# Optimization experiments

Hardware: AMD Instinct MI355X
Metric: run time of the kernel (lower is better)

Reference implementation:

```python
import jax, jax.numpy as jnp
import numpy as np
import math

IMG_SIZE = 768
NUM_CLASSES = 90
THRESHOLD = 0.05
IOU_THRESHOLD = 0.5
MAX_DETECTIONS = 100
K_CAND = 512  # per-class candidate pool before greedy NMS
RATIOS = [(1.0, 1.0), (1.4, 0.7), (0.7, 1.4)]
SCALES = [2 ** 0, 2 ** (1.0 / 3.0), 2 ** (2.0 / 3.0)]


def _generate_anchors():
    anchor_scale = 4.0
    pyramid_levels = [3, 4, 5, 6, 7]
    all_levels = []
    for lv in pyramid_levels:
        stride = 2 ** lv
        size = anchor_scale * 2 ** lv
        grid = IMG_SIZE // stride
        sx = np.arange(grid) * stride
        sy, sx = np.meshgrid(np.arange(grid) * stride, sx, indexing='ij')
        # torch meshgrid(shift_y, shift_x, indexing='ij') -> rows are y
        yy, xx = np.meshgrid(np.arange(grid) * stride, np.arange(grid) * stride, indexing='ij')
        shifts = np.stack([xx.ravel(), yy.ravel(), xx.ravel(), yy.ravel()], axis=1).astype(np.float32)
        base = []
        for r in RATIOS:
            for s in SCALES:
                w = size * s * math.sqrt(r[0] / r[1])
                h = size * s * math.sqrt(r[1] / r[0])
                base.append([-w / 2, -h / 2, w / 2, h / 2])
        base = np.asarray(base, dtype=np.float32)  # [9,4]
        anc = (base[None, :, :] + shifts[:, None, :]).reshape(-1, 4)
        all_levels.append(anc)
    return np.concatenate(all_levels, axis=0)  # [110484,4]


def setup_inputs() -> dict:
    key = jax.random.key(0)
    k1, k2, k3 = jax.random.split(key, 3)
    A = 110484
    x = jax.random.normal(k1, (1, 3, IMG_SIZE, IMG_SIZE), dtype=jnp.float32)
    regression = jax.random.normal(k2, (1, A, 4), dtype=jnp.float32) * 0.3
    classification = jax.random.normal(k3, (1, A, NUM_CLASSES), dtype=jnp.float32) - 2.0
    anchors = jnp.asarray(_generate_anchors())
    return {"x": x, "regression": regression, "classification": classification, "anchors": anchors}


def _decode_and_clip(anchors, deltas, H, W):
    # BBoxTransform (RetinaNet-style): deltas = (dx, dy, dw, dh)
    wa = anchors[:, 2] - anchors[:, 0]
    ha = anchors[:, 3] - anchors[:, 1]
    cxa = anchors[:, 0] + 0.5 * wa
    cya = anchors[:, 1] + 0.5 * ha
    dx, dy, dw, dh = deltas[:, 0], deltas[:, 1], deltas[:, 2], deltas[:, 3]
    cx = cxa + dx * wa
    cy = cya + dy * ha
    w = jnp.exp(dw) * wa
    h = jnp.exp(dh) * ha
    x1 = jnp.clip(cx - 0.5 * w, 0.0, W)
    y1 = jnp.clip(cy - 0.5 * h, 0.0, H)
    x2 = jnp.clip(cx + 0.5 * w, 0.0, W)
    y2 = jnp.clip(cy + 0.5 * h, 0.0, H)
    return jnp.stack([x1, y1, x2, y2], axis=1)  # [A,4]


def _pairwise_iou(b):  # [K,4] -> [K,K]
    area = (b[:, 2] - b[:, 0]) * (b[:, 3] - b[:, 1])
    xx1 = jnp.maximum(b[:, None, 0], b[None, :, 0])
    yy1 = jnp.maximum(b[:, None, 1], b[None, :, 1])
    xx2 = jnp.minimum(b[:, None, 2], b[None, :, 2])
    yy2 = jnp.minimum(b[:, None, 3], b[None, :, 3])
    inter = jnp.clip(xx2 - xx1, 0.0) * jnp.clip(yy2 - yy1, 0.0)
    return inter / (area[:, None] + area[None, :] - inter + 1e-8)


def _greedy_nms(iou_c, valid_c):
    # boxes are pre-sorted by descending score; fixed-iteration greedy NMS
    def step(suppressed, i):
        keep_i = valid_c[i] & jnp.logical_not(suppressed[i])
        suppressed = jnp.where(keep_i, suppressed | (iou_c[i] > IOU_THRESHOLD), suppressed)
        return suppressed, keep_i
    _, keep = jax.lax.scan(step, jnp.zeros(iou_c.shape[0], dtype=bool), jnp.arange(iou_c.shape[0]))
    return keep  # [K]


def _postprocess(x, regression, classification, anchors):
    H, W = x.shape[2], x.shape[3]
    boxes = _decode_and_clip(anchors, regression[0], float(H), float(W))  # [A,4]
    scores = jax.nn.sigmoid(classification[0])                            # [A,C]
    # per-class top-K candidate pool (sorted desc), fixed-shape NMS
    vals, idx = jax.lax.top_k(scores.T, K_CAND)        # [C,K]
    cand = boxes[idx]                                   # [C,K,4]
    valid = vals > THRESHOLD                            # [C,K]
    iou = jax.vmap(_pairwise_iou)(cand)                 # [C,K,K]
    keep = jax.vmap(_greedy_nms)(iou, valid)            # [C,K]
    kept_scores = jnp.where(keep, vals, -1.0).reshape(-1)  # [C*K]
    top_vals, flat_idx = jax.lax.top_k(kept_scores, MAX_DETECTIONS)
    labels = (flat_idx // K_CAND).astype(jnp.float32)
    det_boxes = cand.reshape(-1, 4)[flat_idx]
    ok = top_vals > 0.0
    det = jnp.concatenate([
        jnp.zeros((MAX_DETECTIONS, 1), dtype=jnp.float32),  # batch ids (batch=1 -> 0)
        det_boxes,
        top_vals[:, None],
        labels[:, None],
    ], axis=1)  # [100,7]
    return jnp.where(ok[:, None], det, 0.0)


def reference(x, regression, classification, anchors):
    return _postprocess(x, regression, classification, anchors)
```

## Files before the change

### kernel.cpp

```cpp
#include <hip/hip_runtime.h>
#include <math.h>


#define A_N   110484
#define C_N   90
#define KCAND 512
#define NBINS 8192
#define KSH   19
#define MAXDET 100
#define IMG_F 768.0f
#define THRESH 0.05f
#define NS    4
#define VTOT  (A_N / 4)
#define VS4   ((VTOT + NS - 1) / NS)
#define SL_CAP 1024
#define CAND_N (NS * KCAND)
#define KEEP_CAP 100
#define T_BLKS ((A_N + 63) / 64)
#define S_BLKS (C_N * NS)
#define D_BLKS ((A_N + 255) / 256)
#define FCAP  512

typedef unsigned int u32;
typedef unsigned long long u64;

__device__ __forceinline__ u32 fkey(float f) {
    u32 u = __float_as_uint(f);
    return (u & 0x80000000u) ? ~u : (u | 0x80000000u);
}
__device__ __forceinline__ float unfkey(u32 k) {
    u32 u = (k & 0x80000000u) ? (k ^ 0x80000000u) : ~k;
    return __uint_as_float(u);
}
__device__ __forceinline__ u64 shflx64(u64 v, int m) {
    u32 lo = (u32)__shfl_xor((int)(u32)v, m, 64);
    u32 hi = (u32)__shfl_xor((int)(v >> 32), m, 64);
    return ((u64)hi << 32) | lo;
}

__global__ __launch_bounds__(256)
void prep_kernel(const float* __restrict__ cls,
                 u32* __restrict__ keysT) {
    __shared__ u32 tile[64 * 91];
    const int a0 = blockIdx.x * 64;
    const int lim = min(64, A_N - a0);
    const int n4 = (lim * C_N) >> 2;
    const float4* src4 = (const float4*)(cls + (size_t)a0 * C_N);
    for (int i4 = threadIdx.x; i4 < n4; i4 += 256) {
        float4 x4 = src4[i4];
        const u32 base = (u32)(4 * i4);
        float xs[4] = { x4.x, x4.y, x4.z, x4.w };
        #pragma unroll
        for (int k = 0; k < 4; ++k) {
            u32 i = base + k;
            u32 aa = i / C_N, c = i % C_N;
            float s = 1.0f / (1.0f + expf(-xs[k]));
            tile[aa * 91 + c] = fkey(s);
        }
    }
    __syncthreads();
    for (int j = threadIdx.x; j < C_N * 64; j += 256) {
        int c = j >> 6, aa = j & 63;
        if (aa < lim)
            keysT[(size_t)c * A_N + a0 + aa] = tile[aa * 91 + c];
    }
}

__global__ __launch_bounds__(256)
void select_kernel(const u32* __restrict__ keysT,
                   const float* __restrict__ anchors,
                   const float* __restrict__ reg,
                   float4* __restrict__ boxes,
                   u64* __restrict__ candbuf) {
    __shared__ u32 hist[NBINS];
    __shared__ u32 csum[256];
    __shared__ u64 lbuf[SL_CAP];
    __shared__ u32 sPv;
    __shared__ int lcnt;
    const int tid = threadIdx.x;

    if (blockIdx.x >= S_BLKS) {
        int a = (blockIdx.x - S_BLKS) * 256 + tid;
        if (a < A_N) {
            float4 an = ((const float4*)anchors)[a];
            float4 dl = ((const float4*)reg)[a];
            float wa = an.z - an.x, ha = an.w - an.y;
            float cx = an.x + 0.5f * wa + dl.x * wa;
            float cy = an.y + 0.5f * ha + dl.y * ha;
            float w = expf(dl.z) * wa;
            float h = expf(dl.w) * ha;
            float4 o;
            o.x = fminf(fmaxf(cx - 0.5f * w, 0.0f), IMG_F);
            o.y = fminf(fmaxf(cy - 0.5f * h, 0.0f), IMG_F);
            o.z = fminf(fmaxf(cx + 0.5f * w, 0.0f), IMG_F);
            o.w = fminf(fmaxf(cy + 0.5f * h, 0.0f), IMG_F);
            boxes[a] = o;
        }
        return;
    }
    const int c = blockIdx.x >> 2, s = blockIdx.x & 3;
    const int lo = s * VS4, hiEnd = min(VTOT, lo + VS4);
    const uint4* kv = (const uint4*)(keysT + (size_t)c * A_N);

    for (int i = tid; i < NBINS; i += 256) hist[i] = 0;
    if (tid == 0) { sPv = 0; lcnt = 0; }
    __syncthreads();
    for (int i = lo + tid; i < hiEnd; i += 256) {
        uint4 k = kv[i];
        atomicAdd(&hist[k.x >> KSH], 1u);
        atomicAdd(&hist[k.y >> KSH], 1u);
        atomicAdd(&hist[k.z >> KSH], 1u);
        atomicAdd(&hist[k.w >> KSH], 1u);
    }
    __syncthreads();
    u32 own = 0; const int hi = NBINS - 1 - 32 * tid;
    #pragma unroll 4
    for (int j = 0; j < 32; ++j) own += hist[hi - j];
    csum[tid] = own;
    __syncthreads();
    for (int off = 1; off < 256; off <<= 1) {
        u32 v = csum[tid];
        u32 a = (tid >= off) ? csum[tid - off] : 0u;
        __syncthreads();
        csum[tid] = v + a;
        __syncthreads();
    }
    const u32 incl = csum[tid], excl = incl - own;
    if (excl < (u32)KCAND && incl >= (u32)KCAND) {
        u32 cum = excl;
        for (int j = 0; j < 32; ++j) {
            u32 hv = hist[hi - j];
            if (cum + hv >= (u32)KCAND) { sPv = (u32)(hi - j); break; }
            cum += hv;
        }
    }
    __syncthreads();
    const u32 P = sPv;
    for (int i = lo + tid; i < hiEnd; i += 256) {
        uint4 k = kv[i];
        u32 base = (u32)(4 * i);
        if ((k.x >> KSH) >= P) {
            int p = atomicAdd(&lcnt, 1);
            if (p < SL_CAP) lbuf[p] = (((u64)(~k.x)) << 32) | base;
        }
        if ((k.y >> KSH) >= P) {
            int p = atomicAdd(&lcnt, 1);
            if (p < SL_CAP) lbuf[p] = (((u64)(~k.y)) << 32) | (base + 1);
        }
        if ((k.z >> KSH) >= P) {
            int p = atomicAdd(&lcnt, 1);
            if (p < SL_CAP) lbuf[p] = (((u64)(~k.z)) << 32) | (base + 2);
        }
        if ((k.w >> KSH) >= P) {
            int p = atomicAdd(&lcnt, 1);
            if (p < SL_CAP) lbuf[p] = (((u64)(~k.w)) << 32) | (base + 3);
        }
    }
    __syncthreads();
    const int n = min(lcnt, SL_CAP);
    for (int i = tid; i < SL_CAP; i += 256) if (i >= n) lbuf[i] = ~0ULL;
    __syncthreads();

    {
        const int l = tid & 63, w = tid >> 6;
        int ii[4]; u64 v[4];
        #pragma unroll
        for (int r = 0; r < 4; ++r) { ii[r] = 256 * w + 64 * r + l; v[r] = lbuf[ii[r]]; }
        __syncthreads();
        #pragma unroll
        for (u32 kk = 2; kk <= 1024; kk <<= 1) {
            #pragma unroll
            for (u32 j = kk >> 1; j > 0; j >>= 1) {
                if (j >= 256) {
                    #pragma unroll
                    for (int r = 0; r < 4; ++r) lbuf[ii[r]] = v[r];
                    __syncthreads();
                    #pragma unroll
                    for (int r = 0; r < 4; ++r) {
                        u64 pv = lbuf[ii[r] ^ j];
                        bool up = ((ii[r] & kk) == 0);
                        bool m = (((ii[r] & j) == 0) == up);
                        v[r] = m ? (v[r] < pv ? v[r] : pv) : (v[r] > pv ? v[r] : pv);
                    }
                    __syncthreads();
                } else if (j >= 64) {
                    const int rx = (int)(j >> 6);
                    u64 nv[4];
                    #pragma unroll
                    for (int r = 0; r < 4; ++r) {
                        u64 pv = v[r ^ rx];
                        bool up = ((ii[r] & kk) == 0);
                        bool m = (((ii[r] & j) == 0) == up);
                        nv[r] = m ? (v[r] < pv ? v[r] : pv) : (v[r] > pv ? v[r] : pv);
                    }
                    #pragma unroll
                    for (int r = 0; r < 4; ++r) v[r] = nv[r];
                } else {
                    #pragma unroll
                    for (int r = 0; r < 4; ++r) {
                        u64 pv = shflx64(v[r], (int)j);
                        bool up = ((ii[r] & kk) == 0);
                        bool m = (((ii[r] & j) == 0) == up);
                        v[r] = m ? (v[r] < pv ? v[r] : pv) : (v[r] > pv ? v[r] : pv);
                    }
                }
            }
        }
        u64* cb = candbuf + (size_t)c * CAND_N + (size_t)s * KCAND;
        const bool rev = (s & 1);
        #pragma unroll
        for (int r = 0; r < 4; ++r) {
            if (ii[r] < KCAND) {
                int d = rev ? (KCAND - 1 - ii[r]) : ii[r];
                cb[d] = v[r];
            }
        }
    }
}

__global__ __launch_bounds__(1024)
void snms_kernel(const u64* __restrict__ candbuf,
                 const float4* __restrict__ boxes,
                 u32* __restrict__ keptbuf, u32* __restrict__ cnt2) {
    __shared__ u64 sortbuf[2][CAND_N];
    __shared__ float bxx[KCAND], byy[KCAND], bzz[KCAND], bww[KCAND];
    __shared__ float ar[KCAND], sc[KCAND];
    __shared__ u32 keepf[16], wbase[17];
    u32* bmask = (u32*)&sortbuf[0][0];
    const int c = blockIdx.x, tid = threadIdx.x;
    const int l = tid & 63, w = tid >> 6;
    const int i0 = 128 * w + l, i1 = i0 + 64;

    const u64* cb = candbuf + (size_t)c * CAND_N;
    u64 v0 = cb[i0], v1 = cb[i1];
    int p = 0;
    #pragma unroll
    for (u32 kk = 1024; kk <= (u32)CAND_N; kk <<= 1) {
        #pragma unroll
        for (u32 j = kk >> 1; j > 0; j >>= 1) {
            if (j >= 128) {
                sortbuf[p][i0] = v0; sortbuf[p][i1] = v1;
                __syncthreads();
                u64 w0 = sortbuf[p][i0 ^ j], w1 = sortbuf[p][i1 ^ j];
                bool m0 = (((i0 & j) == 0) == ((i0 & kk) == 0));
                bool m1 = (((i1 & j) == 0) == ((i1 & kk) == 0));
                v0 = m0 ? (v0 < w0 ? v0 : w0) : (v0 > w0 ? v0 : w0);
                v1 = m1 ? (v1 < w1 ? v1 : w1) : (v1 > w1 ? v1 : w1);
                p ^= 1;
            } else if (j == 64) {
                bool up = ((i0 & kk) == 0);
                u64 mn = v0 < v1 ? v0 : v1, mx = v0 < v1 ? v1 : v0;
                v0 = up ? mn : mx; v1 = up ? mx : mn;
            } else {
                u64 w0 = shflx64(v0, (int)j), w1 = shflx64(v1, (int)j);
                bool m0 = (((i0 & j) == 0) == ((i0 & kk) == 0));
                bool m1 = (((i1 & j) == 0) == ((i1 & kk) == 0));
                v0 = m0 ? (v0 < w0 ? v0 : w0) : (v0 > w0 ? v0 : w0);
                v1 = m1 ? (v1 < w1 ? v1 : w1) : (v1 > w1 ? v1 : w1);
            }
        }
    }
    __syncthreads();

    if (w < 4) {
        u32 idx0 = (u32)v0, key0 = ~((u32)(v0 >> 32));
        u32 idx1 = (u32)v1, key1 = ~((u32)(v1 >> 32));
        sc[i0] = unfkey(key0); sc[i1] = unfkey(key1);
        float4 b0 = boxes[idx0], b1 = boxes[idx1];
        bxx[i0] = b0.x; byy[i0] = b0.y; bzz[i0] = b0.z; bww[i0] = b0.w;
        bxx[i1] = b1.x; byy[i1] = b1.y; bzz[i1] = b1.z; bww[i1] = b1.w;
        ar[i0] = (b0.z - b0.x) * (b0.w - b0.y);
        ar[i1] = (b1.z - b1.x) * (b1.w - b1.y);
    }
    for (int i = tid; i < KCAND * 16; i += 1024) bmask[i] = 0;
    if (tid < 16) keepf[tid] = 0;
    __syncthreads();

    {
        const int i = tid & (KCAND - 1);
        const int half = tid >> 9;
        const int count = (KCAND - 1) - i;
        const int j0 = i + 1 + (half ? (count >> 1) : 0);
        const int j1 = half ? KCAND : (i + 1 + (count >> 1));
        const float bix = bxx[i], biy = byy[i], biz = bzz[i], biw = bww[i];
        const float ai = ar[i];
        u32 m[16];
        #pragma unroll
        for (int q = 0; q < 16; ++q) m[q] = 0;
        for (int j = j0; j < j1; ++j) {
            float xx1 = fmaxf(bix, bxx[j]), yy1 = fmaxf(biy, byy[j]);
            float xx2 = fminf(biz, bzz[j]), yy2 = fminf(biw, bww[j]);
            float inter = fmaxf(xx2 - xx1, 0.0f) * fmaxf(yy2 - yy1, 0.0f);
            float uni = ai + ar[j] - inter + 1e-8f;
            if (inter > 0.5f * uni) m[j >> 5] |= (1u << (j & 31));
        }
        #pragma unroll
        for (int q = 0; q < 16; ++q)
            if (m[q]) atomicOr(&bmask[i * 16 + q], m[q]);
    }
    __syncthreads();

    if (tid < 64) {
        const int lw = tid & 15;
        u32 removed = 0, keepw = 0;
        u32 rA[8], rB[8]; float sA[8], sB[8];
        #pragma unroll
        for (int k = 0; k < 8; ++k) { rA[k] = bmask[k * 16 + lw]; sA[k] = sc[k]; }
        #pragma unroll 1
        for (int ch = 0; ch < 64; ch += 2) {
            const int tb1 = (ch + 1) * 8;
            #pragma unroll
            for (int k = 0; k < 8; ++k) { rB[k] = bmask[(tb1 + k) * 16 + lw]; sB[k] = sc[tb1 + k]; }
            {
                const int tb = ch * 8;
                #pragma unroll
                for (int k = 0; k < 8; ++k) {
                    const int t = tb + k;
                    u32 rw = (u32)__builtin_amdgcn_readlane((int)removed, t >> 5);
                    bool d = (sA[k] > THRESH) && (((rw >> (t & 31)) & 1u) == 0u);
                    removed |= d ? rA[k] : 0u;
                    keepw |= (d && (tid == (t >> 5))) ? (1u << (t & 31)) : 0u;
                }
            }
            const int tb2 = (ch + 2 < 64) ? (ch + 2) * 8 : 0;
            #pragma unroll
            for (int k = 0; k < 8; ++k) { rA[k] = bmask[(tb2 + k) * 16 + lw]; sA[k] = sc[tb2 + k]; }
            {
                #pragma unroll
                for (int k = 0; k < 8; ++k) {
                    const int t = tb1 + k;
                    u32 rw = (u32)__builtin_amdgcn_readlane((int)removed, t >> 5);
                    bool d = (sB[k] > THRESH) && (((rw >> (t & 31)) & 1u) == 0u);
                    removed |= d ? rB[k] : 0u;
                    keepw |= (d && (tid == (t >> 5))) ? (1u << (t & 31)) : 0u;
                }
            }
        }
        if (tid < 16) keepf[tid] = keepw;
    }
    __syncthreads();

    if (tid == 0) {
        u32 t = 0;
        for (int q = 0; q < 16; ++q) { wbase[q] = t; t += __popc(keepf[q]); }
        wbase[16] = t;
        cnt2[c] = (t < (u32)KEEP_CAP) ? t : (u32)KEEP_CAP;
    }
    __syncthreads();
    if (tid < KCAND) {
        u32 word = keepf[tid >> 5];
        u32 bit = (u32)tid & 31u;
        if ((word >> bit) & 1u) {
            u32 rank = wbase[tid >> 5] + __popc(word & ((1u << bit) - 1u));
            if (rank < (u32)KEEP_CAP) {
                float s = sc[tid];
                uint4 a, b;
                a.x = ~fkey(s);
                a.y = (u32)(c * KCAND + tid);
                a.z = __float_as_uint(bxx[tid]);
                a.w = __float_as_uint(byy[tid]);
                b.x = __float_as_uint(bzz[tid]);
                b.y = __float_as_uint(bww[tid]);
                b.z = __float_as_uint(s);
                b.w = 0u;
                uint4* e = (uint4*)(keptbuf + ((size_t)c * KEEP_CAP + rank) * 8);
                e[0] = a; e[1] = b;
            }
        }
    }
}

__global__ __launch_bounds__(1024)
void final_kernel(const u32* __restrict__ keptbuf, const u32* __restrict__ cnt2,
                  float* __restrict__ out) {
    __shared__ u32 hist[NBINS];
    __shared__ u32 csum[1024];
    __shared__ u64 ebuf[FCAP];
    __shared__ u32 eidx[FCAP];
    __shared__ u32 scnt[C_N];
    __shared__ u32 sP;
    __shared__ int sN;
    const int tid = threadIdx.x;
    const int TOT = C_N * KEEP_CAP;

    for (int i = tid; i < MAXDET * 7; i += 1024) out[i] = 0.0f;
    for (int i = tid; i < NBINS; i += 1024) hist[i] = 0;
    if (tid < C_N) scnt[tid] = cnt2[tid];
    if (tid == 0) { sN = 0; sP = NBINS - 1; }
    __syncthreads();

    for (int i = tid; i < TOT; i += 1024) {
        u32 c = (u32)i / KEEP_CAP, pp = (u32)i % KEEP_CAP;
        if (pp < scnt[c]) {
            u32 khi = keptbuf[(size_t)i * 8];
            atomicAdd(&hist[khi >> KSH], 1u);
        }
    }
    __syncthreads();
    u32 own = 0; const int lo = 8 * tid;
    #pragma unroll
    for (int j = 0; j < 8; ++j) own += hist[lo + j];
    csum[tid] = own;
    __syncthreads();
    for (int off = 1; off < 1024; off <<= 1) {
        u32 v = csum[tid];
        u32 a = (tid >= off) ? csum[tid - off] : 0u;
        __syncthreads();
        csum[tid] = v + a;
        __syncthreads();
    }
    const u32 incl = csum[tid], excl = incl - own;
    if (excl < (u32)MAXDET && incl >= (u32)MAXDET) {
        u32 cum = excl;
        for (int j = 0; j < 8; ++j) {
            u32 h = hist[lo + j];
            if (cum + h >= (u32)MAXDET) { sP = (u32)(lo + j); break; }
            cum += h;
        }
    }
    __syncthreads();
    const u32 P = sP;
    for (int i = tid; i < TOT; i += 1024) {
        u32 c = (u32)i / KEEP_CAP, pp = (u32)i % KEEP_CAP;
        if (pp < scnt[c]) {
            const uint2 v2 = *((const uint2*)(keptbuf + (size_t)i * 8));
            if ((v2.x >> KSH) <= P) {
                int p = atomicAdd(&sN, 1);
                if (p < FCAP) {
                    ebuf[p] = ((u64)v2.x << 32) | v2.y;
                    eidx[p] = (u32)i;
                }
            }
        }
    }
    __syncthreads();
    const int n = min(sN, FCAP);
    u32 m = 128; while ((int)m < n) m <<= 1;
    for (int i = tid; i < (int)m; i += 1024) if (i >= n) ebuf[i] = ~0ULL;
    __syncthreads();
    for (u32 kk = 2; kk <= m; kk <<= 1) {
        for (u32 j = kk >> 1; j > 0; j >>= 1) {
            u32 i = (u32)tid;
            if (i < m) {
                u32 ixj = i ^ j;
                if (ixj > i) {
                    u64 x = ebuf[i], y = ebuf[ixj];
                    bool up = ((i & kk) == 0);
                    if (up ? (x > y) : (x < y)) {
                        ebuf[i] = y; ebuf[ixj] = x;
                        u32 t = eidx[i]; eidx[i] = eidx[ixj]; eidx[ixj] = t;
                    }
                }
            }
            __syncthreads();
        }
    }
    if (tid < MAXDET && tid < n) {
        u64 comp = ebuf[tid];
        if (comp != ~0ULL) {
            const uint4* e = (const uint4*)(keptbuf + (size_t)eidx[tid] * 8);
            uint4 a = e[0], b = e[1];
            float* o = out + tid * 7;
            o[0] = 0.0f;
            o[1] = __uint_as_float(a.z); o[2] = __uint_as_float(a.w);
            o[3] = __uint_as_float(b.x); o[4] = __uint_as_float(b.y);
            o[5] = __uint_as_float(b.z);
            o[6] = (float)(((u32)comp) >> 9);
        }
    }
}

extern "C" void kernel_launch(void* const* d_in, const int* in_sizes, int n_in,
                              void* d_out, int out_size, void* d_ws, size_t ws_size,
                              hipStream_t stream) {
    const float* reg     = (const float*)d_in[1];
    const float* cls     = (const float*)d_in[2];
    const float* anchors = (const float*)d_in[3];
    float* out = (float*)d_out;

    char* ws = (char*)d_ws;
    size_t off = 0;
    auto alloc = [&](size_t bytes) -> void* {
        void* p = ws + off;
        off = (off + bytes + 255) & ~(size_t)255;
        return p;
    };
    u32*    keysT   = (u32*)   alloc((size_t)C_N * A_N * sizeof(u32));
    float4* boxes   = (float4*)alloc((size_t)A_N * sizeof(float4));
    u64*    candbuf = (u64*)   alloc((size_t)C_N * CAND_N * sizeof(u64));
    u32*    keptbuf = (u32*)   alloc((size_t)C_N * KEEP_CAP * 8 * sizeof(u32));
    u32*    cnt2    = (u32*)   alloc((size_t)C_N * sizeof(u32));
    (void)ws_size;

    prep_kernel<<<T_BLKS, 256, 0, stream>>>(cls, keysT);
    select_kernel<<<S_BLKS + D_BLKS, 256, 0, stream>>>(keysT, anchors, reg, boxes, candbuf);
    snms_kernel<<<C_N, 1024, 0, stream>>>(candbuf, boxes, keptbuf, cnt2);
    final_kernel<<<1, 1024, 0, stream>>>(keptbuf, cnt2, out);
}
```

Before: 217.6 us.

## Widen select blocks, pack histogram into 16-bit halves, ballot-based NMS mask

The select kernel moves from 256 to 512 threads. Its histogram now packs two 16-bit bin counts into each 32-bit shared word, halving LDS usage, and the histogram and compaction loops are unrolled four-wide. The bitonic sort is adapted to two elements per thread. In the NMS kernel, the per-thread IoU loop with atomicOr into the suppression mask is replaced by a wave-per-row layout that builds mask words with __ballot and writes them directly, removing the mask clearing pass and the atomics. The 16-bit counters could overflow if one bin in a slice receives more than 65535 keys.

```diff
diff --git a/kernel.cpp b/kernel.cpp
--- a/kernel.cpp
+++ b/kernel.cpp
@@ -18,7 +18,8 @@
 #define KEEP_CAP 100
 #define T_BLKS ((A_N + 63) / 64)
 #define S_BLKS (C_N * NS)
-#define D_BLKS ((A_N + 255) / 256)
+#define SEL_T 512
+#define D_BLKS ((A_N + SEL_T - 1) / SEL_T)
 #define FCAP  512
 
 typedef unsigned int u32;
@@ -66,21 +67,21 @@
     }
 }
 
-__global__ __launch_bounds__(256)
+__global__ __launch_bounds__(SEL_T)
 void select_kernel(const u32* __restrict__ keysT,
                    const float* __restrict__ anchors,
                    const float* __restrict__ reg,
                    float4* __restrict__ boxes,
                    u64* __restrict__ candbuf) {
-    __shared__ u32 hist[NBINS];
-    __shared__ u32 csum[256];
+    __shared__ u32 hist[NBINS / 2];
+    __shared__ u32 csum[SEL_T];
     __shared__ u64 lbuf[SL_CAP];
     __shared__ u32 sPv;
     __shared__ int lcnt;
     const int tid = threadIdx.x;
 
     if (blockIdx.x >= S_BLKS) {
-        int a = (blockIdx.x - S_BLKS) * 256 + tid;
+        int a = (blockIdx.x - S_BLKS) * SEL_T + tid;
         if (a < A_N) {
             float4 an = ((const float4*)anchors)[a];
             float4 dl = ((const float4*)reg)[a];
@@ -102,23 +103,39 @@
     const int lo = s * VS4, hiEnd = min(VTOT, lo + VS4);
     const uint4* kv = (const uint4*)(keysT + (size_t)c * A_N);
 
-    for (int i = tid; i < NBINS; i += 256) hist[i] = 0;
+    for (int i = tid; i < NBINS / 2; i += SEL_T) hist[i] = 0;
     if (tid == 0) { sPv = 0; lcnt = 0; }
     __syncthreads();
-    for (int i = lo + tid; i < hiEnd; i += 256) {
-        uint4 k = kv[i];
-        atomicAdd(&hist[k.x >> KSH], 1u);
-        atomicAdd(&hist[k.y >> KSH], 1u);
-        atomicAdd(&hist[k.z >> KSH], 1u);
-        atomicAdd(&hist[k.w >> KSH], 1u);
-    }
-    __syncthreads();
-    u32 own = 0; const int hi = NBINS - 1 - 32 * tid;
-    #pragma unroll 4
-    for (int j = 0; j < 32; ++j) own += hist[hi - j];
+
+    #define HACC(K) do { \
+        u32 b0 = (K).x >> KSH, b1 = (K).y >> KSH, b2 = (K).z >> KSH, b3 = (K).w >> KSH; \
+        atomicAdd(&hist[b0 >> 1], 1u << ((b0 & 1) << 4)); \
+        atomicAdd(&hist[b1 >> 1], 1u << ((b1 & 1) << 4)); \
+        atomicAdd(&hist[b2 >> 1], 1u << ((b2 & 1) << 4)); \
+        atomicAdd(&hist[b3 >> 1], 1u << ((b3 & 1) << 4)); } while (0)
+    {
+        int i = lo + tid;
+        for (; i + 3 * SEL_T < hiEnd; i += 4 * SEL_T) {
+            uint4 ka = kv[i], kb = kv[i + SEL_T], kc = kv[i + 2 * SEL_T], kd = kv[i + 3 * SEL_T];
+            HACC(ka); HACC(kb); HACC(kc); HACC(kd);
+        }
+        for (; i < hiEnd; i += SEL_T) { uint4 ka = kv[i]; HACC(ka); }
+    }
+    __syncthreads();
+
+    u32 own = 0;
+    {
+        const int wb = (NBINS / 2) - 8 - 8 * tid;
+        const int g = (tid >> 2) & 7;
+        #pragma unroll
+        for (int jj = 0; jj < 8; ++jj) {
+            u32 v = hist[wb + ((g + jj) & 7)];
+            own += (v & 0xffffu) + (v >> 16);
+        }
+    }
     csum[tid] = own;
     __syncthreads();
-    for (int off = 1; off < 256; off <<= 1) {
+    for (int off = 1; off < SEL_T; off <<= 1) {
         u32 v = csum[tid];
         u32 a = (tid >= off) ? csum[tid - off] : 0u;
         __syncthreads();
@@ -128,100 +145,81 @@
     const u32 incl = csum[tid], excl = incl - own;
     if (excl < (u32)KCAND && incl >= (u32)KCAND) {
         u32 cum = excl;
-        for (int j = 0; j < 32; ++j) {
-            u32 hv = hist[hi - j];
-            if (cum + hv >= (u32)KCAND) { sPv = (u32)(hi - j); break; }
-            cum += hv;
+        const int hb = NBINS - 1 - 16 * tid;
+        for (int j = 0; j < 16; ++j) {
+            int b = hb - j;
+            u32 v = hist[b >> 1];
+            u32 cnt = (b & 1) ? (v >> 16) : (v & 0xffffu);
+            if (cum + cnt >= (u32)KCAND) { sPv = (u32)b; break; }
+            cum += cnt;
         }
     }
     __syncthreads();
     const u32 P = sPv;
-    for (int i = lo + tid; i < hiEnd; i += 256) {
-        uint4 k = kv[i];
-        u32 base = (u32)(4 * i);
-        if ((k.x >> KSH) >= P) {
-            int p = atomicAdd(&lcnt, 1);
-            if (p < SL_CAP) lbuf[p] = (((u64)(~k.x)) << 32) | base;
-        }
-        if ((k.y >> KSH) >= P) {
-            int p = atomicAdd(&lcnt, 1);
-            if (p < SL_CAP) lbuf[p] = (((u64)(~k.y)) << 32) | (base + 1);
-        }
-        if ((k.z >> KSH) >= P) {
-            int p = atomicAdd(&lcnt, 1);
-            if (p < SL_CAP) lbuf[p] = (((u64)(~k.z)) << 32) | (base + 2);
-        }
-        if ((k.w >> KSH) >= P) {
-            int p = atomicAdd(&lcnt, 1);
-            if (p < SL_CAP) lbuf[p] = (((u64)(~k.w)) << 32) | (base + 3);
-        }
+
+    #define CACC(K, BASE) do { \
+        if (((K).x >> KSH) >= P) { int p = atomicAdd(&lcnt, 1); if (p < SL_CAP) lbuf[p] = (((u64)(~(K).x)) << 32) | (u32)(BASE); } \
+        if (((K).y >> KSH) >= P) { int p = atomicAdd(&lcnt, 1); if (p < SL_CAP) lbuf[p] = (((u64)(~(K).y)) << 32) | (u32)((BASE) + 1); } \
+        if (((K).z >> KSH) >= P) { int p = atomicAdd(&lcnt, 1); if (p < SL_CAP) lbuf[p] = (((u64)(~(K).z)) << 32) | (u32)((BASE) + 2); } \
+        if (((K).w >> KSH) >= P) { int p = atomicAdd(&lcnt, 1); if (p < SL_CAP) lbuf[p] = (((u64)(~(K).w)) << 32) | (u32)((BASE) + 3); } } while (0)
+    {
+        int i = lo + tid;
+        for (; i + 3 * SEL_T < hiEnd; i += 4 * SEL_T) {
+            uint4 ka = kv[i], kb = kv[i + SEL_T], kc = kv[i + 2 * SEL_T], kd = kv[i + 3 * SEL_T];
+            CACC(ka, 4 * i); CACC(kb, 4 * (i + SEL_T)); CACC(kc, 4 * (i + 2 * SEL_T)); CACC(kd, 4 * (i + 3 * SEL_T));
+        }
+        for (; i < hiEnd; i += SEL_T) { uint4 ka = kv[i]; CACC(ka, 4 * i); }
     }
     __syncthreads();
     const int n = min(lcnt, SL_CAP);
-    for (int i = tid; i < SL_CAP; i += 256) if (i >= n) lbuf[i] = ~0ULL;
+    for (int q = tid; q < SL_CAP; q += SEL_T) if (q >= n) lbuf[q] = ~0ULL;
     __syncthreads();
 
     {
         const int l = tid & 63, w = tid >> 6;
-        int ii[4]; u64 v[4];
-        #pragma unroll
-        for (int r = 0; r < 4; ++r) { ii[r] = 256 * w + 64 * r + l; v[r] = lbuf[ii[r]]; }
+        const int i0 = 128 * w + l, i1 = i0 + 64;
+        u64 v0 = lbuf[i0], v1 = lbuf[i1];
         __syncthreads();
         #pragma unroll
         for (u32 kk = 2; kk <= 1024; kk <<= 1) {
             #pragma unroll
             for (u32 j = kk >> 1; j > 0; j >>= 1) {
-                if (j >= 256) {
-                    #pragma unroll
-                    for (int r = 0; r < 4; ++r) lbuf[ii[r]] = v[r];
+                if (j >= 128) {
+                    lbuf[i0] = v0; lbuf[i1] = v1;
                     __syncthreads();
-                    #pragma unroll
-                    for (int r = 0; r < 4; ++r) {
-                        u64 pv = lbuf[ii[r] ^ j];
-                        bool up = ((ii[r] & kk) == 0);
-                        bool m = (((ii[r] & j) == 0) == up);
-                        v[r] = m ? (v[r] < pv ? v[r] : pv) : (v[r] > pv ? v[r] : pv);
-                    }
+                    u64 w0 = lbuf[i0 ^ j], w1 = lbuf[i1 ^ j];
+                    bool m0 = (((i0 & j) == 0) == ((i0 & kk) == 0));
+                    bool m1 = (((i1 & j) == 0) == ((i1 & kk) == 0));
+                    v0 = m0 ? (v0 < w0 ? v0 : w0) : (v0 > w0 ? v0 : w0);
+                    v1 = m1 ? (v1 < w1 ? v1 : w1) : (v1 > w1 ? v1 : w1);
                     __syncthreads();
-                } else if (j >= 64) {
-                    const int rx = (int)(j >> 6);
-                    u64 nv[4];
-                    #pragma unroll
-                    for (int r = 0; r < 4; ++r) {
-                        u64 pv = v[r ^ rx];
-                        bool up = ((ii[r] & kk) == 0);
-                        bool m = (((ii[r] & j) == 0) == up);
-                        nv[r] = m ? (v[r] < pv ? v[r] : pv) : (v[r] > pv ? v[r] : pv);
-                    }
-                    #pragma unroll
-                    for (int r = 0; r < 4; ++r) v[r] = nv[r];
+                } else if (j == 64) {
+                    bool up = ((i0 & kk) == 0);
+                    u64 mn = v0 < v1 ? v0 : v1, mx = v0 < v1 ? v1 : v0;
+                    v0 = up ? mn : mx; v1 = up ? mx : mn;
                 } else {
-                    #pragma unroll
-                    for (int r = 0; r < 4; ++r) {
-                        u64 pv = shflx64(v[r], (int)j);
-                        bool up = ((ii[r] & kk) == 0);
-                        bool m = (((ii[r] & j) == 0) == up);
-                        v[r] = m ? (v[r] < pv ? v[r] : pv) : (v[r] > pv ? v[r] : pv);
-                    }
+                    u64 w0 = shflx64(v0, (int)j), w1 = shflx64(v1, (int)j);
+                    bool m0 = (((i0 & j) == 0) == ((i0 & kk) == 0));
+                    bool m1 = (((i1 & j) == 0) == ((i1 & kk) == 0));
+                    v0 = m0 ? (v0 < w0 ? v0 : w0) : (v0 > w0 ? v0 : w0);
+                    v1 = m1 ? (v1 < w1 ? v1 : w1) : (v1 > w1 ? v1 : w1);
                 }
             }
         }
-        u64* cb = candbuf + (size_t)c * CAND_N + (size_t)s * KCAND;
-        const bool rev = (s & 1);
-        #pragma unroll
-        for (int r = 0; r < 4; ++r) {
-            if (ii[r] < KCAND) {
-                int d = rev ? (KCAND - 1 - ii[r]) : ii[r];
-                cb[d] = v[r];
-            }
+        if (w < 4) {
+            u64* cb = candbuf + (size_t)c * CAND_N + (size_t)s * KCAND;
+            const bool rev = (s & 1);
+            int d0 = rev ? (KCAND - 1 - i0) : i0;
+            int d1 = rev ? (KCAND - 1 - i1) : i1;
+            cb[d0] = v0; cb[d1] = v1;
         }
     }
 }
 
 __global__ __launch_bounds__(1024)
-void snms_kernel(const u64* __restrict__ candbuf,
-                 const float4* __restrict__ boxes,
-                 u32* __restrict__ keptbuf, u32* __restrict__ cnt2) {
+void nms_kernel(const u64* __restrict__ candbuf,
+                const float4* __restrict__ boxes,
+                u32* __restrict__ keptbuf, u32* __restrict__ cnt2) {
     __shared__ u64 sortbuf[2][CAND_N];
     __shared__ float bxx[KCAND], byy[KCAND], bzz[KCAND], bww[KCAND];
     __shared__ float ar[KCAND], sc[KCAND];
@@ -272,31 +270,26 @@
         ar[i0] = (b0.z - b0.x) * (b0.w - b0.y);
         ar[i1] = (b1.z - b1.x) * (b1.w - b1.y);
     }
-    for (int i = tid; i < KCAND * 16; i += 1024) bmask[i] = 0;
     if (tid < 16) keepf[tid] = 0;
     __syncthreads();
 
-    {
-        const int i = tid & (KCAND - 1);
-        const int half = tid >> 9;
-        const int count = (KCAND - 1) - i;
-        const int j0 = i + 1 + (half ? (count >> 1) : 0);
-        const int j1 = half ? KCAND : (i + 1 + (count >> 1));
-        const float bix = bxx[i], biy = byy[i], biz = bzz[i], biw = bww[i];
-        const float ai = ar[i];
-        u32 m[16];
-        #pragma unroll
-        for (int q = 0; q < 16; ++q) m[q] = 0;
-        for (int j = j0; j < j1; ++j) {
+    for (int r = w; r < KCAND; r += 16) {
+        const float bix = bxx[r], biy = byy[r], biz = bzz[r], biw = bww[r];
+        const float ai = ar[r];
+        const int q0 = (r + 1) >> 6;
+        u32* row = bmask + r * 16;
+        if (l < 2 * q0) row[l] = 0;
+        for (int q = q0; q < 8; ++q) {
+            const int j = q * 64 + l;
             float xx1 = fmaxf(bix, bxx[j]), yy1 = fmaxf(biy, byy[j]);
             float xx2 = fminf(biz, bzz[j]), yy2 = fminf(biw, bww[j]);
             float inter = fmaxf(xx2 - xx1, 0.0f) * fmaxf(yy2 - yy1, 0.0f);
             float uni = ai + ar[j] - inter + 1e-8f;
-            if (inter > 0.5f * uni) m[j >> 5] |= (1u << (j & 31));
-        }
-        #pragma unroll
-        for (int q = 0; q < 16; ++q)
-            if (m[q]) atomicOr(&bmask[i * 16 + q], m[q]);
+            bool sup = (j > r) && (inter > 0.5f * uni);
+            u64 bal = __ballot(sup);
+            if (l == 0)      row[2 * q]     = (u32)bal;
+            else if (l == 1) row[2 * q + 1] = (u32)(bal >> 32);
+        }
     }
     __syncthreads();
 
@@ -493,7 +486,7 @@
     (void)ws_size;
 
     prep_kernel<<<T_BLKS, 256, 0, stream>>>(cls, keysT);
-    select_kernel<<<S_BLKS + D_BLKS, 256, 0, stream>>>(keysT, anchors, reg, boxes, candbuf);
-    snms_kernel<<<C_N, 1024, 0, stream>>>(candbuf, boxes, keptbuf, cnt2);
+    select_kernel<<<S_BLKS + D_BLKS, SEL_T, 0, stream>>>(keysT, anchors, reg, boxes, candbuf);
+    nms_kernel<<<C_N, 1024, 0, stream>>>(candbuf, boxes, keptbuf, cnt2);
     final_kernel<<<1, 1024, 0, stream>>>(keptbuf, cnt2, out);
 }
```

After: 210.0 us. 1.04x faster.
